# Kernel optimization log

Measured on AMD Instinct MI355X. Metric: run time of the kernel, lower is better.

The kernel has to match this reference:

```python
import jax, jax.numpy as jnp
import numpy as np

DIM = 1024
NUM_HEADS = 16
HEAD_DIM = DIM // NUM_HEADS
N_PREFIX = 5
SCALE = HEAD_DIM ** -0.5


def _rotate_half(x):
    h = x.shape[-1] // 2
    return jnp.concatenate([-x[..., h:], x[..., :h]], axis=-1)


def _apply_rope(x, cos, sin):
    return x * cos + _rotate_half(x) * sin


def setup_inputs() -> dict:
    key = jax.random.key(0)
    ks = jax.random.split(key, 12)
    B, S = 8, N_PREFIX + 1024
    x = jax.random.normal(ks[0], (B, S, DIM), dtype=jnp.float32)
    rope_cos = jax.random.uniform(ks[1], (1024, HEAD_DIM), dtype=jnp.float32)
    rope_sin = jax.random.uniform(ks[2], (1024, HEAD_DIM), dtype=jnp.float32)
    sd = DIM ** -0.5
    Wq = jax.random.normal(ks[3], (DIM, DIM), dtype=jnp.float32) * sd
    bq = jnp.zeros((DIM,), dtype=jnp.float32)
    Wk = jax.random.normal(ks[4], (DIM, DIM), dtype=jnp.float32) * sd
    Wv = jax.random.normal(ks[5], (DIM, DIM), dtype=jnp.float32) * sd
    bv = jnp.zeros((DIM,), dtype=jnp.float32)
    Wo = jax.random.normal(ks[6], (DIM, DIM), dtype=jnp.float32) * sd
    bo = jnp.zeros((DIM,), dtype=jnp.float32)
    return {"x": x, "rope_cos": rope_cos, "rope_sin": rope_sin,
            "Wq": Wq, "bq": bq, "Wk": Wk, "Wv": Wv, "bv": bv,
            "Wo": Wo, "bo": bo}


def reference(x, rope_cos, rope_sin, Wq, bq, Wk, Wv, bv, Wo, bo):
    B, S, D = x.shape
    # projections: Q and V have bias, K has no bias
    q = (x @ Wq + bq).reshape(B, S, NUM_HEADS, HEAD_DIM).transpose(0, 2, 1, 3)
    k = (x @ Wk).reshape(B, S, NUM_HEADS, HEAD_DIM).transpose(0, 2, 1, 3)
    v = (x @ Wv + bv).reshape(B, S, NUM_HEADS, HEAD_DIM).transpose(0, 2, 1, 3)
    # 2D RoPE on patch tokens only (prefix tokens untouched)
    cos = rope_cos[None, None]  # [1,1,P,hd]
    sin = rope_sin[None, None]
    q = jnp.concatenate([q[:, :, :N_PREFIX], _apply_rope(q[:, :, N_PREFIX:], cos, sin)], axis=2)
    k = jnp.concatenate([k[:, :, :N_PREFIX], _apply_rope(k[:, :, N_PREFIX:], cos, sin)], axis=2)
    q = q * SCALE
    attn = jax.nn.softmax(jnp.einsum('bhqd,bhkd->bhqk', q, k), axis=-1)
    out = jnp.einsum('bhqk,bhkd->bhqd', attn, v)
    out = out.transpose(0, 2, 1, 3).reshape(B, S, D)
    return out @ Wo + bo
```

## Files before the change

kernel.cpp:

```cpp
#include <hip/hip_runtime.h>

typedef unsigned short u16;
typedef __bf16 bf16x8 __attribute__((ext_vector_type(8)));
typedef unsigned short u16x8 __attribute__((ext_vector_type(8)));
typedef float f32x4 __attribute__((ext_vector_type(4)));

#define M_ROWS 8232
#define SEQ 1029
#define NPREF 5
#define DIMN 1024
#define NH 16
#define HD 64

#define GP(p) ((__attribute__((address_space(1))) void*)(unsigned long long)(const void*)(p))
#define LP(p) ((__attribute__((address_space(3))) void*)(unsigned)(unsigned long long)(const void*)(p))

#define BAR_VM4  asm volatile("s_waitcnt vmcnt(4)\ns_barrier" ::: "memory")
#define BAR_VM0  asm volatile("s_waitcnt vmcnt(0)\ns_barrier" ::: "memory")
#define BAR_LGKM asm volatile("s_waitcnt lgkmcnt(0)\ns_barrier" ::: "memory")

__device__ __forceinline__ u16 f2bf(float f) {
  unsigned u = __float_as_uint(f);
  u += 0x7fffu + ((u >> 16) & 1u);
  return (u16)(u >> 16);
}

__device__ __forceinline__ unsigned pk2bf(float lo, float hi) {
  unsigned ul = __float_as_uint(lo);
  unsigned uh = __float_as_uint(hi);
  ul += 0x7fffu + ((ul >> 16) & 1u);
  uh += 0x7fffu + ((uh >> 16) & 1u);
  return __builtin_amdgcn_perm(uh, ul, 0x07060302u);
}

__global__ __launch_bounds__(256) void k_cvt_x(const float* __restrict__ x, u16* __restrict__ xb) {
  size_t i = ((size_t)blockIdx.x * 256 + threadIdx.x) * 4;
  float4 v = *reinterpret_cast<const float4*>(x + i);
  ushort4 o;
  o.x = f2bf(v.x); o.y = f2bf(v.y); o.z = f2bf(v.z); o.w = f2bf(v.w);
  *reinterpret_cast<ushort4*>(xb + i) = o;
}

__global__ __launch_bounds__(256) void k_wt(const float* __restrict__ W0, const float* __restrict__ W1,
                                            const float* __restrict__ W2, const float* __restrict__ W3,
                                            u16* __restrict__ T0, u16* __restrict__ T1,
                                            u16* __restrict__ T2, u16* __restrict__ T3) {
  const float* W; u16* T;
  switch (blockIdx.z) {
    case 0: W = W0; T = T0; break;
    case 1: W = W1; T = T1; break;
    case 2: W = W2; T = T2; break;
    default: W = W3; T = T3; break;
  }
  __shared__ float tile[32][33];
  int tx = threadIdx.x & 31, ty = threadIdx.x >> 5;
  int k0 = blockIdx.x * 32, n0 = blockIdx.y * 32;
#pragma unroll
  for (int j = 0; j < 4; ++j)
    tile[ty + j * 8][tx] = W[(size_t)(k0 + ty + j * 8) * DIMN + n0 + tx];
  __syncthreads();
#pragma unroll
  for (int j = 0; j < 4; ++j)
    T[(size_t)(n0 + ty + j * 8) * DIMN + k0 + tx] = f2bf(tile[tx][ty + j * 8]);
}

__global__ __launch_bounds__(256) void k_qkv(
    const u16* __restrict__ Xb,
    const u16* __restrict__ WqT, const u16* __restrict__ WkT, const u16* __restrict__ WvT,
    const float* __restrict__ bq, const float* __restrict__ bv,
    const float* __restrict__ rc, const float* __restrict__ rs,
    u16* __restrict__ Qg, u16* __restrict__ Kg, u16* __restrict__ Vg)
{
  int bid = blockIdx.x;
  int rxcd = bid & 7, tt = bid >> 3;
  int mq = tt / 24, j24 = tt - mq * 24;
  int mt = mq * 8 + rxcd;
  if (mt >= 65) return;
  int mode = j24 >> 3, nt = j24 & 7;
  const u16* WT = (mode == 0) ? WqT : (mode == 1) ? WkT : WvT;
  u16* dst = (mode == 0) ? Qg : (mode == 1) ? Kg : Vg;
  int m0 = mt * 128, n0 = nt * 128;

  __shared__ u16 Al[2][128 * 32];
  __shared__ u16 Bl[2][128 * 32];

  int t = threadIdx.x, lane = t & 63, wv = t >> 6;
  int fr = lane & 15, quad = lane >> 4;
  int wm = (wv >> 1) * 64, wn = (wv & 1) * 64;

  int srow = lane >> 2;
  int scol = (lane & 3) * 8;
  int ar0 = m0 + wv * 32 + srow; if (ar0 >= M_ROWS) ar0 = M_ROWS - 1;
  int ar1 = m0 + wv * 32 + 16 + srow; if (ar1 >= M_ROWS) ar1 = M_ROWS - 1;
  int br0 = n0 + wv * 32 + srow;
  int br1 = br0 + 16;
  const u16* agp0 = Xb + (size_t)ar0 * DIMN + scol;
  const u16* agp1 = Xb + (size_t)ar1 * DIMN + scol;
  const u16* bgp0 = WT + (size_t)br0 * DIMN + scol;
  const u16* bgp1 = WT + (size_t)br1 * DIMN + scol;

#define QKV_ISSUE(koff, bb) do { \
    __builtin_amdgcn_global_load_lds(GP(agp0 + (koff)), LP(&Al[bb][wv * 1024]), 16, 0, 0); \
    __builtin_amdgcn_global_load_lds(GP(agp1 + (koff)), LP(&Al[bb][wv * 1024 + 512]), 16, 0, 0); \
    __builtin_amdgcn_global_load_lds(GP(bgp0 + (koff)), LP(&Bl[bb][wv * 1024]), 16, 0, 0); \
    __builtin_amdgcn_global_load_lds(GP(bgp1 + (koff)), LP(&Bl[bb][wv * 1024 + 512]), 16, 0, 0); \
  } while (0)

  f32x4 zero4 = {0.f, 0.f, 0.f, 0.f};
  f32x4 acc[4][4];
#pragma unroll
  for (int i = 0; i < 4; ++i)
#pragma unroll
    for (int j = 0; j < 4; ++j) acc[i][j] = zero4;

  QKV_ISSUE(0, 0);
  QKV_ISSUE(32, 1);
  for (int kk = 0; kk < 32; ++kk) {
    int bb = kk & 1;
    if (kk < 31) { BAR_VM4; } else { BAR_VM0; }
    bf16x8 af[4], bfr[4];
#pragma unroll
    for (int i = 0; i < 4; ++i)
      af[i] = *reinterpret_cast<const bf16x8*>(&Al[bb][(wm + i * 16 + fr) * 32 + quad * 8]);
#pragma unroll
    for (int j = 0; j < 4; ++j)
      bfr[j] = *reinterpret_cast<const bf16x8*>(&Bl[bb][(wn + j * 16 + fr) * 32 + quad * 8]);
#pragma unroll
    for (int i = 0; i < 4; ++i)
#pragma unroll
      for (int j = 0; j < 4; ++j)
        acc[i][j] = __builtin_amdgcn_mfma_f32_16x16x32_bf16(af[i], bfr[j], acc[i][j], 0, 0, 0);
    if (kk < 30) {
      BAR_LGKM;
      QKV_ISSUE((kk + 2) * 32, bb);
    }
  }

  int h = (n0 + wn) >> 6;
#pragma unroll
  for (int i = 0; i < 4; ++i) {
    int rowbase = m0 + wm + i * 16 + quad * 4;
#pragma unroll
    for (int r = 0; r < 4; ++r) {
      int row = rowbase + r;
      if (row >= M_ROWS) continue;
      int b = row / SEQ;
      int s = row - b * SEQ;
#pragma unroll
      for (int j = 0; j < 4; ++j) {
        int d = j * 16 + fr;
        float v = acc[i][j][r];
        float outv;
        if (mode == 2) {
          outv = v + bv[n0 + wn + d];
        } else {
          float vb = v;
          int jp = j ^ 2;
          float pv = acc[i][jp][r];
          if (mode == 0) {
            vb += bq[n0 + wn + d];
            pv += bq[n0 + wn + (jp * 16 + fr)];
          }
          if (s >= NPREF) {
            int p = s - NPREF;
            float c = rc[p * HD + d];
            float sn = rs[p * HD + d];
            float rot = (d < 32) ? -pv : pv;
            outv = vb * c + rot * sn;
          } else {
            outv = vb;
          }
          if (mode == 0) outv *= 0.125f;
        }
        dst[((size_t)(b * NH + h) * SEQ + s) * HD + d] = f2bf(outv);
      }
    }
  }
}

__global__ __launch_bounds__(256) void k_attn(
    const u16* __restrict__ Qg, const u16* __restrict__ Kg, const u16* __restrict__ Vg,
    u16* __restrict__ AO)
{
  int bh = blockIdx.x;
  int q0 = blockIdx.y * 128;
  int b = bh >> 4, h = bh & 15;
  const size_t base = (size_t)bh * SEQ * HD;

  __shared__ u16 Ks[64 * 72];
  __shared__ u16 Vt[64 * 72];
  __shared__ u16 Ps[4][32 * 72];

  int t = threadIdx.x, lane = t & 63, wv = t >> 6;
  int fr = lane & 15, quad = lane >> 4;

  int ki = t >> 2;
  int kc0 = (t & 3) * 16;
  int vs0 = (t & 31) * 2;
  int vdo = (t >> 5) * 8;

  bf16x8 qf[2][2];
#pragma unroll
  for (int qt = 0; qt < 2; ++qt) {
#pragma unroll
    for (int st = 0; st < 2; ++st) {
      int row = q0 + wv * 32 + qt * 16 + fr;
      if (row >= SEQ) row = SEQ - 1;
      qf[qt][st] = *reinterpret_cast<const bf16x8*>(Qg + base + (size_t)row * HD + st * 32 + quad * 8);
    }
  }

  u16x8 one16 = {0x3F80, 0x3F80, 0x3F80, 0x3F80, 0x3F80, 0x3F80, 0x3F80, 0x3F80};
  bf16x8 vone = __builtin_bit_cast(bf16x8, one16);

  f32x4 zero4 = {0.f, 0.f, 0.f, 0.f};
  f32x4 o[2][5];
#pragma unroll
  for (int qt = 0; qt < 2; ++qt)
#pragma unroll
    for (int di = 0; di < 5; ++di) o[qt][di] = zero4;

  uint4 krA0, krA1, vrA0, vrA1;
  {
    int kr = ki; if (kr >= SEQ) kr = SEQ - 1;
    const u16* ksrc = Kg + base + (size_t)kr * HD;
    krA0 = *reinterpret_cast<const uint4*>(ksrc + kc0);
    krA1 = *reinterpret_cast<const uint4*>(ksrc + kc0 + 8);
    int r0 = vs0; if (r0 >= SEQ) r0 = SEQ - 1;
    int r1 = vs0 + 1; if (r1 >= SEQ) r1 = SEQ - 1;
    vrA0 = *reinterpret_cast<const uint4*>(Vg + base + (size_t)r0 * HD + vdo);
    vrA1 = *reinterpret_cast<const uint4*>(Vg + base + (size_t)r1 * HD + vdo);
  }

  for (int kt = 0; kt < 17; ++kt) {
    int k0 = kt * 64;
    BAR_LGKM;
    *reinterpret_cast<uint4*>(&Ks[ki * 72 + kc0]) = krA0;
    *reinterpret_cast<uint4*>(&Ks[ki * 72 + kc0 + 8]) = krA1;
    {
      u16 v0[8], v1[8];
      *reinterpret_cast<uint4*>(v0) = vrA0;
      *reinterpret_cast<uint4*>(v1) = vrA1;
#pragma unroll
      for (int j = 0; j < 8; ++j) {
        unsigned pk = (unsigned)v0[j] | ((unsigned)v1[j] << 16);
        *reinterpret_cast<unsigned*>(&Vt[(vdo + j) * 72 + vs0]) = pk;
      }
    }
    if (kt < 16) {
      int kn = k0 + 64;
      int kr = kn + ki; if (kr >= SEQ) kr = SEQ - 1;
      const u16* ksrc = Kg + base + (size_t)kr * HD;
      krA0 = *reinterpret_cast<const uint4*>(ksrc + kc0);
      krA1 = *reinterpret_cast<const uint4*>(ksrc + kc0 + 8);
      int r0 = kn + vs0; if (r0 >= SEQ) r0 = SEQ - 1;
      int r1 = kn + vs0 + 1; if (r1 >= SEQ) r1 = SEQ - 1;
      vrA0 = *reinterpret_cast<const uint4*>(Vg + base + (size_t)r0 * HD + vdo);
      vrA1 = *reinterpret_cast<const uint4*>(Vg + base + (size_t)r1 * HD + vdo);
    }
    BAR_LGKM;

    f32x4 sc[4][2];
#pragma unroll
    for (int mi = 0; mi < 4; ++mi)
#pragma unroll
      for (int qt = 0; qt < 2; ++qt) sc[mi][qt] = zero4;
#pragma unroll
    for (int st = 0; st < 2; ++st) {
#pragma unroll
      for (int mi = 0; mi < 4; ++mi) {
        bf16x8 kf = *reinterpret_cast<const bf16x8*>(&Ks[(mi * 16 + fr) * 72 + st * 32 + quad * 8]);
#pragma unroll
        for (int qt = 0; qt < 2; ++qt)
          sc[mi][qt] = __builtin_amdgcn_mfma_f32_16x16x32_bf16(kf, qf[qt][st], sc[mi][qt], 0, 0, 0);
      }
    }

    bool last = (kt == 16);
#pragma unroll
    for (int qt = 0; qt < 2; ++qt) {
#pragma unroll
      for (int mi = 0; mi < 4; ++mi) {
        float p0, p1, p2, p3;
        {
          float s0v = sc[mi][qt][0], s1v = sc[mi][qt][1], s2v = sc[mi][qt][2], s3v = sc[mi][qt][3];
          if (last) {
            int kc = mi * 16 + quad * 4;
            if (kc + 0 >= NPREF) s0v = -1e30f;
            if (kc + 1 >= NPREF) s1v = -1e30f;
            if (kc + 2 >= NPREF) s2v = -1e30f;
            if (kc + 3 >= NPREF) s3v = -1e30f;
          }
          p0 = __expf(s0v - 16.0f);
          p1 = __expf(s1v - 16.0f);
          p2 = __expf(s2v - 16.0f);
          p3 = __expf(s3v - 16.0f);
        }
        unsigned d0 = pk2bf(p0, p1);
        unsigned d1 = pk2bf(p2, p3);
        uint2 w; w.x = d0; w.y = d1;
        *reinterpret_cast<uint2*>(&Ps[wv][(qt * 16 + fr) * 72 + mi * 16 + quad * 4]) = w;
      }
    }

#pragma unroll
    for (int st = 0; st < 2; ++st) {
      bf16x8 pf[2];
#pragma unroll
      for (int qt = 0; qt < 2; ++qt)
        pf[qt] = *reinterpret_cast<const bf16x8*>(&Ps[wv][(qt * 16 + fr) * 72 + st * 32 + quad * 8]);
#pragma unroll
      for (int di = 0; di < 4; ++di) {
        bf16x8 vf = *reinterpret_cast<const bf16x8*>(&Vt[(di * 16 + fr) * 72 + st * 32 + quad * 8]);
#pragma unroll
        for (int qt = 0; qt < 2; ++qt)
          o[qt][di] = __builtin_amdgcn_mfma_f32_16x16x32_bf16(pf[qt], vf, o[qt][di], 0, 0, 0);
      }
#pragma unroll
      for (int qt = 0; qt < 2; ++qt)
        o[qt][4] = __builtin_amdgcn_mfma_f32_16x16x32_bf16(pf[qt], vone, o[qt][4], 0, 0, 0);
    }
  }

#pragma unroll
  for (int qt = 0; qt < 2; ++qt) {
#pragma unroll
    for (int r = 0; r < 4; ++r) {
      int srow = q0 + wv * 32 + qt * 16 + quad * 4 + r;
      if (srow >= SEQ) continue;
      float inv = 1.f / o[qt][4][r];
#pragma unroll
      for (int di = 0; di < 4; ++di) {
        float v = o[qt][di][r] * inv;
        AO[((size_t)b * SEQ + srow) * DIMN + h * HD + di * 16 + fr] = f2bf(v);
      }
    }
  }
}

__global__ __launch_bounds__(256) void k_out(
    const u16* __restrict__ Ab, const u16* __restrict__ WoT,
    const float* __restrict__ bo, float* __restrict__ Out)
{
  int bid = blockIdx.x;
  int rxcd = bid & 7, tt = bid >> 3;
  int mq = tt >> 3, nt = tt & 7;
  int mt = mq * 8 + rxcd;
  if (mt >= 65) return;
  int m0 = mt * 128, n0 = nt * 128;

  __shared__ u16 Al[2][128 * 32];
  __shared__ u16 Bl[2][128 * 32];

  int t = threadIdx.x, lane = t & 63, wv = t >> 6;
  int fr = lane & 15, quad = lane >> 4;
  int wm = (wv >> 1) * 64, wn = (wv & 1) * 64;

  int srow = lane >> 2;
  int scol = (lane & 3) * 8;
  int ar0 = m0 + wv * 32 + srow; if (ar0 >= M_ROWS) ar0 = M_ROWS - 1;
  int ar1 = m0 + wv * 32 + 16 + srow; if (ar1 >= M_ROWS) ar1 = M_ROWS - 1;
  int br0 = n0 + wv * 32 + srow;
  int br1 = br0 + 16;
  const u16* agp0 = Ab + (size_t)ar0 * DIMN + scol;
  const u16* agp1 = Ab + (size_t)ar1 * DIMN + scol;
  const u16* bgp0 = WoT + (size_t)br0 * DIMN + scol;
  const u16* bgp1 = WoT + (size_t)br1 * DIMN + scol;

#define OUT_ISSUE(koff, bb) do { \
    __builtin_amdgcn_global_load_lds(GP(agp0 + (koff)), LP(&Al[bb][wv * 1024]), 16, 0, 0); \
    __builtin_amdgcn_global_load_lds(GP(agp1 + (koff)), LP(&Al[bb][wv * 1024 + 512]), 16, 0, 0); \
    __builtin_amdgcn_global_load_lds(GP(bgp0 + (koff)), LP(&Bl[bb][wv * 1024]), 16, 0, 0); \
    __builtin_amdgcn_global_load_lds(GP(bgp1 + (koff)), LP(&Bl[bb][wv * 1024 + 512]), 16, 0, 0); \
  } while (0)

  f32x4 zero4 = {0.f, 0.f, 0.f, 0.f};
  f32x4 acc[4][4];
#pragma unroll
  for (int i = 0; i < 4; ++i)
#pragma unroll
    for (int j = 0; j < 4; ++j) acc[i][j] = zero4;

  OUT_ISSUE(0, 0);
  OUT_ISSUE(32, 1);
  for (int kk = 0; kk < 32; ++kk) {
    int bb = kk & 1;
    if (kk < 31) { BAR_VM4; } else { BAR_VM0; }
    bf16x8 af[4], bfr[4];
#pragma unroll
    for (int i = 0; i < 4; ++i)
      af[i] = *reinterpret_cast<const bf16x8*>(&Al[bb][(wm + i * 16 + fr) * 32 + quad * 8]);
#pragma unroll
    for (int j = 0; j < 4; ++j)
      bfr[j] = *reinterpret_cast<const bf16x8*>(&Bl[bb][(wn + j * 16 + fr) * 32 + quad * 8]);
#pragma unroll
    for (int i = 0; i < 4; ++i)
#pragma unroll
      for (int j = 0; j < 4; ++j)
        acc[i][j] = __builtin_amdgcn_mfma_f32_16x16x32_bf16(af[i], bfr[j], acc[i][j], 0, 0, 0);
    if (kk < 30) {
      BAR_LGKM;
      OUT_ISSUE((kk + 2) * 32, bb);
    }
  }

#pragma unroll
  for (int i = 0; i < 4; ++i) {
    int rowbase = m0 + wm + i * 16 + quad * 4;
#pragma unroll
    for (int r = 0; r < 4; ++r) {
      int row = rowbase + r;
      if (row >= M_ROWS) continue;
#pragma unroll
      for (int j = 0; j < 4; ++j) {
        int col = n0 + wn + j * 16 + fr;
        Out[(size_t)row * DIMN + col] = acc[i][j][r] + bo[col];
      }
    }
  }
}

extern "C" void kernel_launch(void* const* d_in, const int* in_sizes, int n_in,
                              void* d_out, int out_size, void* d_ws, size_t ws_size,
                              hipStream_t stream)
{
  const float* x  = (const float*)d_in[0];
  const float* rc = (const float*)d_in[1];
  const float* rs = (const float*)d_in[2];
  const float* Wq = (const float*)d_in[3];
  const float* bq = (const float*)d_in[4];
  const float* Wk = (const float*)d_in[5];
  const float* Wv = (const float*)d_in[6];
  const float* bv = (const float*)d_in[7];
  const float* Wo = (const float*)d_in[8];
  const float* bo = (const float*)d_in[9];
  float* Out = (float*)d_out;

  u16* p = (u16*)d_ws;
  u16* Xb  = p; p += (size_t)M_ROWS * DIMN;
  u16* WqT = p; p += (size_t)DIMN * DIMN;
  u16* WkT = p; p += (size_t)DIMN * DIMN;
  u16* WvT = p; p += (size_t)DIMN * DIMN;
  u16* WoT = p; p += (size_t)DIMN * DIMN;
  u16* Qg  = p; p += (size_t)M_ROWS * DIMN;
  u16* Kg  = p; p += (size_t)M_ROWS * DIMN;
  u16* Vg  = p; p += (size_t)M_ROWS * DIMN;
  u16* AO  = p; p += (size_t)M_ROWS * DIMN;

  k_cvt_x<<<M_ROWS, 256, 0, stream>>>(x, Xb);
  dim3 gt(32, 32, 4);
  k_wt<<<gt, 256, 0, stream>>>(Wq, Wk, Wv, Wo, WqT, WkT, WvT, WoT);
  k_qkv<<<1728, 256, 0, stream>>>(Xb, WqT, WkT, WvT, bq, bv, rc, rs, Qg, Kg, Vg);
  dim3 g2(128, 9);
  k_attn<<<g2, 256, 0, stream>>>(Qg, Kg, Vg, AO);
  k_out<<<576, 256, 0, stream>>>(AO, WoT, bo, Out);
}
```

Before: 340.6 us.

## Replace LDS-staged GEMM tiles with direct global-to-register fragment loads and prefetch

The QKV and output projection GEMMs stop staging A/B tiles through shared memory with global_load_lds and barriers. Each lane now loads its MFMA fragments straight from global memory into registers, prefetching the next k-step one iteration ahead. The block-to-tile mapping drops the XCD-aware swizzle and the wasted early-exit blocks, giving an exact grid size. This removes barriers and LDS traffic, but each wave now fetches its operands separately, so tiles shared between waves are read twice from global memory or cache, with narrower and less coalesced access.

```diff
diff --git a/kernel.cpp b/kernel.cpp
--- a/kernel.cpp
+++ b/kernel.cpp
@@ -12,11 +12,6 @@
 #define NH 16
 #define HD 64
 
-#define GP(p) ((__attribute__((address_space(1))) void*)(unsigned long long)(const void*)(p))
-#define LP(p) ((__attribute__((address_space(3))) void*)(unsigned)(unsigned long long)(const void*)(p))
-
-#define BAR_VM4  asm volatile("s_waitcnt vmcnt(4)\ns_barrier" ::: "memory")
-#define BAR_VM0  asm volatile("s_waitcnt vmcnt(0)\ns_barrier" ::: "memory")
 #define BAR_LGKM asm volatile("s_waitcnt lgkmcnt(0)\ns_barrier" ::: "memory")
 
 __device__ __forceinline__ u16 f2bf(float f) {
@@ -72,39 +67,27 @@
     u16* __restrict__ Qg, u16* __restrict__ Kg, u16* __restrict__ Vg)
 {
   int bid = blockIdx.x;
-  int rxcd = bid & 7, tt = bid >> 3;
-  int mq = tt / 24, j24 = tt - mq * 24;
-  int mt = mq * 8 + rxcd;
-  if (mt >= 65) return;
-  int mode = j24 >> 3, nt = j24 & 7;
+  int nt = bid & 7;
+  int tmp = bid >> 3;
+  int mt = tmp % 65;
+  int mode = tmp / 65;
   const u16* WT = (mode == 0) ? WqT : (mode == 1) ? WkT : WvT;
   u16* dst = (mode == 0) ? Qg : (mode == 1) ? Kg : Vg;
   int m0 = mt * 128, n0 = nt * 128;
 
-  __shared__ u16 Al[2][128 * 32];
-  __shared__ u16 Bl[2][128 * 32];
-
   int t = threadIdx.x, lane = t & 63, wv = t >> 6;
   int fr = lane & 15, quad = lane >> 4;
   int wm = (wv >> 1) * 64, wn = (wv & 1) * 64;
 
-  int srow = lane >> 2;
-  int scol = (lane & 3) * 8;
-  int ar0 = m0 + wv * 32 + srow; if (ar0 >= M_ROWS) ar0 = M_ROWS - 1;
-  int ar1 = m0 + wv * 32 + 16 + srow; if (ar1 >= M_ROWS) ar1 = M_ROWS - 1;
-  int br0 = n0 + wv * 32 + srow;
-  int br1 = br0 + 16;
-  const u16* agp0 = Xb + (size_t)ar0 * DIMN + scol;
-  const u16* agp1 = Xb + (size_t)ar1 * DIMN + scol;
-  const u16* bgp0 = WT + (size_t)br0 * DIMN + scol;
-  const u16* bgp1 = WT + (size_t)br1 * DIMN + scol;
-
-#define QKV_ISSUE(koff, bb) do { \
-    __builtin_amdgcn_global_load_lds(GP(agp0 + (koff)), LP(&Al[bb][wv * 1024]), 16, 0, 0); \
-    __builtin_amdgcn_global_load_lds(GP(agp1 + (koff)), LP(&Al[bb][wv * 1024 + 512]), 16, 0, 0); \
-    __builtin_amdgcn_global_load_lds(GP(bgp0 + (koff)), LP(&Bl[bb][wv * 1024]), 16, 0, 0); \
-    __builtin_amdgcn_global_load_lds(GP(bgp1 + (koff)), LP(&Bl[bb][wv * 1024 + 512]), 16, 0, 0); \
-  } while (0)
+  const u16* ap[4];
+  const u16* bp[4];
+#pragma unroll
+  for (int i = 0; i < 4; ++i) {
+    int arow = m0 + wm + i * 16 + fr; if (arow >= M_ROWS) arow = M_ROWS - 1;
+    ap[i] = Xb + (size_t)arow * DIMN + quad * 8;
+    int brow = n0 + wn + i * 16 + fr;
+    bp[i] = WT + (size_t)brow * DIMN + quad * 8;
+  }
 
   f32x4 zero4 = {0.f, 0.f, 0.f, 0.f};
   f32x4 acc[4][4];
@@ -113,27 +96,29 @@
 #pragma unroll
     for (int j = 0; j < 4; ++j) acc[i][j] = zero4;
 
-  QKV_ISSUE(0, 0);
-  QKV_ISSUE(32, 1);
-  for (int kk = 0; kk < 32; ++kk) {
-    int bb = kk & 1;
-    if (kk < 31) { BAR_VM4; } else { BAR_VM0; }
-    bf16x8 af[4], bfr[4];
+  bf16x8 ac[4], bc[4], an[4], bn[4];
+#pragma unroll
+  for (int i = 0; i < 4; ++i) {
+    ac[i] = *reinterpret_cast<const bf16x8*>(ap[i]);
+    bc[i] = *reinterpret_cast<const bf16x8*>(bp[i]);
+  }
+
+#pragma unroll 2
+  for (int k0 = 0; k0 < DIMN; k0 += 32) {
+    if (k0 < DIMN - 32) {
+#pragma unroll
+      for (int i = 0; i < 4; ++i) {
+        an[i] = *reinterpret_cast<const bf16x8*>(ap[i] + k0 + 32);
+        bn[i] = *reinterpret_cast<const bf16x8*>(bp[i] + k0 + 32);
+      }
+    }
 #pragma unroll
     for (int i = 0; i < 4; ++i)
-      af[i] = *reinterpret_cast<const bf16x8*>(&Al[bb][(wm + i * 16 + fr) * 32 + quad * 8]);
-#pragma unroll
-    for (int j = 0; j < 4; ++j)
-      bfr[j] = *reinterpret_cast<const bf16x8*>(&Bl[bb][(wn + j * 16 + fr) * 32 + quad * 8]);
-#pragma unroll
-    for (int i = 0; i < 4; ++i)
 #pragma unroll
       for (int j = 0; j < 4; ++j)
-        acc[i][j] = __builtin_amdgcn_mfma_f32_16x16x32_bf16(af[i], bfr[j], acc[i][j], 0, 0, 0);
-    if (kk < 30) {
-      BAR_LGKM;
-      QKV_ISSUE((kk + 2) * 32, bb);
-    }
+        acc[i][j] = __builtin_amdgcn_mfma_f32_16x16x32_bf16(ac[i], bc[j], acc[i][j], 0, 0, 0);
+#pragma unroll
+    for (int i = 0; i < 4; ++i) { ac[i] = an[i]; bc[i] = bn[i]; }
   }
 
   int h = (n0 + wn) >> 6;
@@ -343,36 +328,23 @@
     const float* __restrict__ bo, float* __restrict__ Out)
 {
   int bid = blockIdx.x;
-  int rxcd = bid & 7, tt = bid >> 3;
-  int mq = tt >> 3, nt = tt & 7;
-  int mt = mq * 8 + rxcd;
-  if (mt >= 65) return;
+  int nt = bid & 7;
+  int mt = bid >> 3;
   int m0 = mt * 128, n0 = nt * 128;
-
-  __shared__ u16 Al[2][128 * 32];
-  __shared__ u16 Bl[2][128 * 32];
 
   int t = threadIdx.x, lane = t & 63, wv = t >> 6;
   int fr = lane & 15, quad = lane >> 4;
   int wm = (wv >> 1) * 64, wn = (wv & 1) * 64;
 
-  int srow = lane >> 2;
-  int scol = (lane & 3) * 8;
-  int ar0 = m0 + wv * 32 + srow; if (ar0 >= M_ROWS) ar0 = M_ROWS - 1;
-  int ar1 = m0 + wv * 32 + 16 + srow; if (ar1 >= M_ROWS) ar1 = M_ROWS - 1;
-  int br0 = n0 + wv * 32 + srow;
-  int br1 = br0 + 16;
-  const u16* agp0 = Ab + (size_t)ar0 * DIMN + scol;
-  const u16* agp1 = Ab + (size_t)ar1 * DIMN + scol;
-  const u16* bgp0 = WoT + (size_t)br0 * DIMN + scol;
-  const u16* bgp1 = WoT + (size_t)br1 * DIMN + scol;
-
-#define OUT_ISSUE(koff, bb) do { \
-    __builtin_amdgcn_global_load_lds(GP(agp0 + (koff)), LP(&Al[bb][wv * 1024]), 16, 0, 0); \
-    __builtin_amdgcn_global_load_lds(GP(agp1 + (koff)), LP(&Al[bb][wv * 1024 + 512]), 16, 0, 0); \
-    __builtin_amdgcn_global_load_lds(GP(bgp0 + (koff)), LP(&Bl[bb][wv * 1024]), 16, 0, 0); \
-    __builtin_amdgcn_global_load_lds(GP(bgp1 + (koff)), LP(&Bl[bb][wv * 1024 + 512]), 16, 0, 0); \
-  } while (0)
+  const u16* ap[4];
+  const u16* bp[4];
+#pragma unroll
+  for (int i = 0; i < 4; ++i) {
+    int arow = m0 + wm + i * 16 + fr; if (arow >= M_ROWS) arow = M_ROWS - 1;
+    ap[i] = Ab + (size_t)arow * DIMN + quad * 8;
+    int brow = n0 + wn + i * 16 + fr;
+    bp[i] = WoT + (size_t)brow * DIMN + quad * 8;
+  }
 
   f32x4 zero4 = {0.f, 0.f, 0.f, 0.f};
   f32x4 acc[4][4];
@@ -381,27 +353,29 @@
 #pragma unroll
     for (int j = 0; j < 4; ++j) acc[i][j] = zero4;
 
-  OUT_ISSUE(0, 0);
-  OUT_ISSUE(32, 1);
-  for (int kk = 0; kk < 32; ++kk) {
-    int bb = kk & 1;
-    if (kk < 31) { BAR_VM4; } else { BAR_VM0; }
-    bf16x8 af[4], bfr[4];
+  bf16x8 ac[4], bc[4], an[4], bn[4];
+#pragma unroll
+  for (int i = 0; i < 4; ++i) {
+    ac[i] = *reinterpret_cast<const bf16x8*>(ap[i]);
+    bc[i] = *reinterpret_cast<const bf16x8*>(bp[i]);
+  }
+
+#pragma unroll 2
+  for (int k0 = 0; k0 < DIMN; k0 += 32) {
+    if (k0 < DIMN - 32) {
+#pragma unroll
+      for (int i = 0; i < 4; ++i) {
+        an[i] = *reinterpret_cast<const bf16x8*>(ap[i] + k0 + 32);
+        bn[i] = *reinterpret_cast<const bf16x8*>(bp[i] + k0 + 32);
+      }
+    }
 #pragma unroll
     for (int i = 0; i < 4; ++i)
-      af[i] = *reinterpret_cast<const bf16x8*>(&Al[bb][(wm + i * 16 + fr) * 32 + quad * 8]);
-#pragma unroll
-    for (int j = 0; j < 4; ++j)
-      bfr[j] = *reinterpret_cast<const bf16x8*>(&Bl[bb][(wn + j * 16 + fr) * 32 + quad * 8]);
-#pragma unroll
-    for (int i = 0; i < 4; ++i)
 #pragma unroll
       for (int j = 0; j < 4; ++j)
-        acc[i][j] = __builtin_amdgcn_mfma_f32_16x16x32_bf16(af[i], bfr[j], acc[i][j], 0, 0, 0);
-    if (kk < 30) {
-      BAR_LGKM;
-      OUT_ISSUE((kk + 2) * 32, bb);
-    }
+        acc[i][j] = __builtin_amdgcn_mfma_f32_16x16x32_bf16(ac[i], bc[j], acc[i][j], 0, 0, 0);
+#pragma unroll
+    for (int i = 0; i < 4; ++i) { ac[i] = an[i]; bc[i] = bn[i]; }
   }
 
 #pragma unroll
@@ -450,8 +424,8 @@
   k_cvt_x<<<M_ROWS, 256, 0, stream>>>(x, Xb);
   dim3 gt(32, 32, 4);
   k_wt<<<gt, 256, 0, stream>>>(Wq, Wk, Wv, Wo, WqT, WkT, WvT, WoT);
-  k_qkv<<<1728, 256, 0, stream>>>(Xb, WqT, WkT, WvT, bq, bv, rc, rs, Qg, Kg, Vg);
+  k_qkv<<<1560, 256, 0, stream>>>(Xb, WqT, WkT, WvT, bq, bv, rc, rs, Qg, Kg, Vg);
   dim3 g2(128, 9);
   k_attn<<<g2, 256, 0, stream>>>(Qg, Kg, Vg, AO);
-  k_out<<<576, 256, 0, stream>>>(AO, WoT, bo, Out);
-}
+  k_out<<<520, 256, 0, stream>>>(AO, WoT, bo, Out);
+}
```

Result: slower. 504.5 us (+48.1%).
